# Kernel optimization log

Hardware: AMD Instinct MI355X
Metric: run time of the kernel (lower is better)

The kernel has to match this reference:

```python
import jax, jax.numpy as jnp
import numpy as np
from jax import lax

G = 8      # deform groups (weight groups == offset groups)
K = 3      # kernel size
K2 = K * K


def conv3x3(x, w, b):
    # NCHW, 3x3, stride 1, padding 1 (SAME)
    y = lax.conv_general_dilated(x, w, (1, 1), 'SAME',
                                 dimension_numbers=('NCHW', 'OIHW', 'NCHW'))
    return y + b[None, :, None, None]


def deform_conv2d(ref, offsets, w, b):
    # ref: [B,C,H,W], offsets: [B,2*G*K2,H,W] (torchvision layout: per group,
    # per kernel position, (dy, dx) pairs), w: [C_out, C_in/G, K, K], b: [C_out]
    B, C, H, W = ref.shape
    Cg = C // G
    off = offsets.reshape(B, G, K2, 2, H, W)
    dy = off[:, :, :, 0]  # [B,G,K2,H,W]
    dx = off[:, :, :, 1]
    ky = (jnp.arange(K2) // K - K // 2).astype(ref.dtype)  # kernel y offsets (pad=1)
    kx = (jnp.arange(K2) % K - K // 2).astype(ref.dtype)
    base_y = jnp.arange(H, dtype=ref.dtype)[:, None] + ky[:, None, None]  # [K2,H,1]
    base_x = jnp.arange(W, dtype=ref.dtype)[None, :] + kx[:, None, None]  # [K2,1,W]
    py = dy + base_y  # [B,G,K2,H,W]
    px = dx + base_x

    y0 = jnp.floor(py).astype(jnp.int32)
    x0 = jnp.floor(px).astype(jnp.int32)
    ly = py - y0.astype(ref.dtype)
    lx = px - x0.astype(ref.dtype)

    ref_flat = ref.reshape(B, G, Cg, H * W)

    def gather(yi, xi):
        valid = (yi >= 0) & (yi < H) & (xi >= 0) & (xi < W)
        idx = jnp.clip(yi, 0, H - 1) * W + jnp.clip(xi, 0, W - 1)  # [B,G,K2,H,W]
        vals = jnp.take_along_axis(ref_flat, idx.reshape(B, G, 1, K2 * H * W), axis=3)
        vals = vals.reshape(B, G, Cg, K2, H, W)
        return vals * valid[:, :, None].astype(ref.dtype)

    w00 = ((1 - ly) * (1 - lx))[:, :, None]
    w01 = ((1 - ly) * lx)[:, :, None]
    w10 = (ly * (1 - lx))[:, :, None]
    w11 = (ly * lx)[:, :, None]
    sampled = (w00 * gather(y0, x0) + w01 * gather(y0, x0 + 1)
               + w10 * gather(y0 + 1, x0) + w11 * gather(y0 + 1, x0 + 1))
    # grouped accumulation: weight [C_out, Cg, K, K] -> [G, OCg, Cg, K2]
    wg = w.reshape(G, C // G, Cg, K2)
    out = jnp.einsum('bgikhw,goik->bgohw', sampled, wg)
    return out.reshape(B, C, H, W) + b[None, :, None, None]


def setup_inputs() -> dict:
    key = jax.random.key(0)
    ks = jax.random.split(key, 10)
    B, C, H, W = 2, 64, 256, 256
    s64 = 1.0 / np.sqrt(C * 9)
    s128 = 1.0 / np.sqrt(128 * 9)
    return {
        'offset': jax.random.normal(ks[0], (B, C, H, W), jnp.float32),
        'ref': jax.random.normal(ks[1], (B, C, H, W), jnp.float32),
        'w_off': jax.random.normal(ks[2], (2 * K2 * G, C, K, K), jnp.float32) * s64,
        'b_off': jnp.zeros((2 * K2 * G,), jnp.float32),
        'w_def': jax.random.normal(ks[3], (C, C // G, K, K), jnp.float32) * (1.0 / np.sqrt((C // G) * 9)),
        'b_def': jnp.zeros((C,), jnp.float32),
        'w_r1': jax.random.normal(ks[4], (C, 2 * C, K, K), jnp.float32) * s128,
        'b_r1': jnp.zeros((C,), jnp.float32),
        'w_r2': jax.random.normal(ks[5], (C, C, K, K), jnp.float32) * s64,
        'b_r2': jnp.zeros((C,), jnp.float32),
    }


def reference(offset, ref, w_off, b_off, w_def, b_def, w_r1, b_r1, w_r2, b_r2):
    deform_offsets = conv3x3(offset, w_off, b_off)              # [B,144,H,W]
    aligned_ref = deform_conv2d(ref, deform_offsets, w_def, b_def)
    x = jnp.concatenate([ref, aligned_ref], axis=1)             # [B,128,H,W]
    x = jax.nn.relu(conv3x3(x, w_r1, b_r1))
    x = jax.nn.relu(conv3x3(x, w_r2, b_r2))
    return x + aligned_ref
```

## Files before the change

### kernel.cpp

```cpp
#include <hip/hip_runtime.h>

typedef __attribute__((ext_vector_type(8)))  short  short8;
typedef __attribute__((ext_vector_type(4)))  float  float4v;
typedef __attribute__((ext_vector_type(16))) float  float16v;

constexpr int HH = 256, WW = 256;
constexpr int PD = 258;
constexpr size_t HWsz = (size_t)HH * WW;

__device__ inline unsigned short f2bf(float f) {
    unsigned int u = __builtin_bit_cast(unsigned int, f);
    u += 0x7FFFu + ((u >> 16) & 1u);
    return (unsigned short)(u >> 16);
}
__device__ inline float bfhalf(unsigned int w, int hi) {
    return __builtin_bit_cast(float, hi ? (w & 0xFFFF0000u) : (w << 16));
}

template<int CDST, bool WRITE_G>
__global__ __launch_bounds__(256) void nchw_to_nhwc(
    const float* __restrict__ src, unsigned short* __restrict__ dst,
    unsigned short* __restrict__ dst_g)
{
    const int px = threadIdx.x, h = blockIdx.x, bi = blockIdx.y;
    const float* s = src + (size_t)bi * 64 * HWsz + (size_t)h * WW + px;
    unsigned short* d = dst + (((size_t)bi * PD + (h + 1)) * PD + (px + 1)) * CDST;
#pragma unroll
    for (int cg = 0; cg < 8; ++cg) {
        float v[8];
#pragma unroll
        for (int j = 0; j < 8; ++j) v[j] = s[(size_t)(cg * 8 + j) * HWsz];
        uint4 pk;
        pk.x = f2bf(v[0]) | ((unsigned)f2bf(v[1]) << 16);
        pk.y = f2bf(v[2]) | ((unsigned)f2bf(v[3]) << 16);
        pk.z = f2bf(v[4]) | ((unsigned)f2bf(v[5]) << 16);
        pk.w = f2bf(v[6]) | ((unsigned)f2bf(v[7]) << 16);
        *(uint4*)&d[cg * 8] = pk;
        if (WRITE_G) {
            unsigned short* dg = dst_g +
                (((size_t)(bi * 8 + cg) * HWsz) + (size_t)h * WW + px) * 8;
            *(uint4*)dg = pk;
        }
    }
}

__global__ __launch_bounds__(256) void zero_border(
    unsigned short* __restrict__ p_off, unsigned short* __restrict__ p_cat,
    unsigned short* __restrict__ p_x1)
{
    const int bi = blockIdx.y, which = blockIdx.z;
    unsigned short* buf = which == 0 ? p_off : (which == 1 ? p_cat : p_x1);
    const int CIN = (which == 1) ? 128 : 64;
    const int NG = CIN / 8;
    unsigned short* p = buf + (size_t)bi * PD * PD * CIN;
    const int total = 1028 * 16;
    for (int i = blockIdx.x * 256 + threadIdx.x; i < total; i += gridDim.x * 256) {
        int g = i & 15;
        if (g >= NG) continue;
        int pxi = i >> 4;
        int r, c;
        if (pxi < 258)       { r = 0;   c = pxi; }
        else if (pxi < 516)  { r = 257; c = pxi - 258; }
        else if (pxi < 772)  { r = pxi - 516 + 1; c = 0; }
        else                 { r = pxi - 772 + 1; c = 257; }
        uint4 z = {0, 0, 0, 0};
        *(uint4*)&p[((size_t)r * PD + c) * CIN + g * 8] = z;
    }
}

__device__ inline void pack_one(const float* __restrict__ w, short* __restrict__ wpk,
                                int Cout, int Cin, int e)
{
    int j = e & 7;
    int lane = (e >> 3) & 63;
    int ksp = 9 * (Cin / 16);
    int kstep = (e >> 9) % ksp;
    int cot = (e >> 9) / ksp;
    int tap = kstep / (Cin / 16);
    int ci = (kstep % (Cin / 16)) * 16 + (lane >> 5) * 8 + j;
    int co = cot * 32 + (lane & 31);
    float v = (co < Cout) ? w[((size_t)co * Cin + ci) * 9 + tap] : 0.f;
    wpk[e] = (short)f2bf(v);
}

__global__ __launch_bounds__(256) void pack_all(
    const float* __restrict__ w1, short* __restrict__ d1,
    const float* __restrict__ w2, short* __restrict__ d2,
    const float* __restrict__ w3, short* __restrict__ d3)
{
    int e = blockIdx.x * 256 + threadIdx.x;
    if (e < 110592)               pack_one(w1, d1, 144, 64, e);
    else if (e < 110592 + 73728)  pack_one(w2, d2, 64, 128, e - 110592);
    else if (e < 221184)          pack_one(w3, d3, 64, 64,  e - 184320);
}

template<int CIN, int COF, int COTB, int MODE, int MINW>
__global__ __launch_bounds__(256, MINW) void conv_mfma_nb(
    const unsigned short* __restrict__ src,
    const short* __restrict__ wpk,
    const float* __restrict__ bias,
    unsigned short* __restrict__ dst_bf,
    float* __restrict__ dst_f,
    const unsigned short* __restrict__ resid_bf)
{
    constexpr int CHUNKS = CIN / 32;
    constexpr int KST = 9 * (CIN / 16);
    constexpr int WSEG = 3 * 4 * 66 * 8;

    __shared__ unsigned short lds[4 * WSEG];

    const int tid  = threadIdx.x;
    const int lane = tid & 63;
    const int wv   = tid >> 6;
    const int half = lane >> 5;
    const int n32  = lane & 31;
    const int h  = blockIdx.x;
    const int bi = blockIdx.y / COTB;
    const int cb = blockIdx.y % COTB;
    const int cbase = cb * COF * 32;

    unsigned short* my = lds + wv * WSEG;
    const unsigned short* srcB = src + (size_t)bi * PD * PD * CIN;
    const short8* wbase = (const short8*)wpk;

    float16v acc[COF][2];
#pragma unroll
    for (int f = 0; f < COF; ++f) {
        float16v bv;
#pragma unroll
        for (int reg = 0; reg < 16; ++reg) {
            int co = cbase + f * 32 + (reg >> 2) * 8 + 4 * half + (reg & 3);
            float b = 0.f;
            if (MODE != 0 || co < 144) b = bias[co];
            bv[reg] = b;
        }
        acc[f][0] = bv;
        acc[f][1] = bv;
    }

    for (int ch = 0; ch < CHUNKS; ++ch) {
        const unsigned short* gband = srcB + ((size_t)h * PD + wv * 64) * CIN + ch * 32;
#pragma unroll
        for (int i0 = 0; i0 < 264; i0 += 64) {
            int i = i0 + lane;
            if (i0 + 64 > 264 && i >= 264) continue;
            int px = i >> 2, o = i & 3;
#pragma unroll
            for (int r = 0; r < 3; ++r) {
                uint4 v = *(const uint4*)(gband + ((size_t)r * PD + px) * CIN + o * 8);
                *(uint4*)&my[(((size_t)r * 4 + o) * 66 + px) * 8] = v;
            }
        }

#pragma unroll
        for (int tap = 0; tap < 9; ++tap) {
            const int row = tap / 3, dxo = tap % 3;
#pragma unroll
            for (int s = 0; s < 2; ++s) {
                const int kstep = tap * (CIN / 16) + ch * 2 + s;
                short8 a[COF];
#pragma unroll
                for (int f = 0; f < COF; ++f)
                    a[f] = wbase[((size_t)(cb * COF + f) * KST + kstep) * 64 + lane];
#pragma unroll
                for (int nt = 0; nt < 2; ++nt) {
                    short8 b = *(const short8*)
                        &my[(((size_t)row * 4 + s * 2 + half) * 66 + nt * 32 + dxo + n32) * 8];
#pragma unroll
                    for (int f = 0; f < COF; ++f)
                        acc[f][nt] = __builtin_amdgcn_mfma_f32_32x32x16_bf16(a[f], b, acc[f][nt], 0, 0, 0);
                }
            }
        }
    }

#pragma unroll
    for (int f = 0; f < COF; ++f) {
#pragma unroll
        for (int nt = 0; nt < 2; ++nt) {
            const int px = wv * 64 + nt * 32 + n32;
            float16v a = acc[f][nt];
#pragma unroll
            for (int q = 0; q < 4; ++q) {
                const int co4 = cbase + f * 32 + q * 8 + 4 * half;
                float v0 = a[q * 4 + 0], v1 = a[q * 4 + 1];
                float v2 = a[q * 4 + 2], v3 = a[q * 4 + 3];
                if (MODE == 0) {
                    if (co4 < 144) {
                        unsigned short* d = dst_bf + (size_t)bi * HWsz * 144;
                        uint2 pk;
                        pk.x = f2bf(v0) | ((unsigned)f2bf(v1) << 16);
                        pk.y = f2bf(v2) | ((unsigned)f2bf(v3) << 16);
                        *(uint2*)&d[((size_t)h * WW + px) * 144 + co4] = pk;
                    }
                } else if (MODE == 1) {
                    unsigned short* d = dst_bf + (size_t)bi * PD * PD * 64;
                    uint2 pk;
                    pk.x = f2bf(fmaxf(v0, 0.f)) | ((unsigned)f2bf(fmaxf(v1, 0.f)) << 16);
                    pk.y = f2bf(fmaxf(v2, 0.f)) | ((unsigned)f2bf(fmaxf(v3, 0.f)) << 16);
                    *(uint2*)&d[(((size_t)h + 1) * PD + (px + 1)) * 64 + co4] = pk;
                } else {
                    const unsigned short* rp = resid_bf + (size_t)bi * PD * PD * 128;
                    uint2 rv = *(const uint2*)&rp[(((size_t)h + 1) * PD + (px + 1)) * 128 + 64 + co4];
                    float r0 = bfhalf(rv.x, 0), r1 = bfhalf(rv.x, 1);
                    float r2 = bfhalf(rv.y, 0), r3 = bfhalf(rv.y, 1);
                    float* d = dst_f + (size_t)bi * 64 * HWsz + (size_t)h * WW + px;
                    d[(size_t)(co4 + 0) * HWsz] = fmaxf(v0, 0.f) + r0;
                    d[(size_t)(co4 + 1) * HWsz] = fmaxf(v1, 0.f) + r1;
                    d[(size_t)(co4 + 2) * HWsz] = fmaxf(v2, 0.f) + r2;
                    d[(size_t)(co4 + 3) * HWsz] = fmaxf(v3, 0.f) + r3;
                }
            }
        }
    }
}

__global__ __launch_bounds__(256) void deform_k6(
    const unsigned short* __restrict__ refg,
    const unsigned short* __restrict__ doff,
    const float* __restrict__ wdef, const float* __restrict__ bdef,
    unsigned short* __restrict__ pcat_out)
{
    __shared__ float wsm2[576];
    const int L = blockIdx.x;
    const int xcd = L & 7;
    const int j = L >> 3;
    const int g = j & 7;
    const int r = (j >> 3) & 31;
    const int bi = j >> 8;
    const int h = xcd * 32 + r;
    const int px = threadIdx.x;

    for (int i = threadIdx.x; i < 576; i += 256) {
        int o = i & 7, c = (i >> 3) & 7, k = i >> 6;
        wsm2[i] = wdef[(size_t)g * 576 + o * 72 + c * 9 + k];
    }
    __syncthreads();

    const unsigned int* dp = (const unsigned int*)(
        doff + (((size_t)bi * HWsz) + (size_t)h * WW + px) * 144 + g * 18);
    unsigned int dw[9];
#pragma unroll
    for (int k = 0; k < 9; ++k) dw[k] = dp[k];

    float2 acc2[4];
#pragma unroll
    for (int o = 0; o < 4; ++o)
        acc2[o] = make_float2(bdef[g * 8 + 2 * o], bdef[g * 8 + 2 * o + 1]);

    const unsigned short* rb = refg + (size_t)(bi * 8 + g) * HWsz * 8;

#pragma unroll
    for (int k = 0; k < 9; ++k) {
        float dy = bfhalf(dw[k], 0);
        float dx = bfhalf(dw[k], 1);
        float py = dy + (float)(h + k / 3 - 1);
        float pxs = dx + (float)(px + k % 3 - 1);
        float fy = floorf(py), fx = floorf(pxs);
        int y0 = (int)fy, x0i = (int)fx;
        float ly = py - fy, lx = pxs - fx;
        int y1 = y0 + 1, x1i = x0i + 1;
        bool vy0 = (y0 >= 0) & (y0 < HH), vy1 = (y1 >= 0) & (y1 < HH);
        bool vx0 = (x0i >= 0) & (x0i < WW), vx1 = (x1i >= 0) & (x1i < WW);
        int cy0 = min(max(y0, 0), HH - 1), cy1 = min(max(y1, 0), HH - 1);
        int cx0 = min(max(x0i, 0), WW - 1), cx1 = min(max(x1i, 0), WW - 1);
        float w00 = (1.f - ly) * (1.f - lx), w01 = (1.f - ly) * lx;
        float w10 = ly * (1.f - lx), w11 = ly * lx;
        if (!(vy0 && vx0)) w00 = 0.f;
        if (!(vy0 && vx1)) w01 = 0.f;
        if (!(vy1 && vx0)) w10 = 0.f;
        if (!(vy1 && vx1)) w11 = 0.f;

        uint4 q00 = *(const uint4*)(rb + ((size_t)cy0 * WW + cx0) * 8);
        uint4 q01 = *(const uint4*)(rb + ((size_t)cy0 * WW + cx1) * 8);
        uint4 q10 = *(const uint4*)(rb + ((size_t)cy1 * WW + cx0) * 8);
        uint4 q11 = *(const uint4*)(rb + ((size_t)cy1 * WW + cx1) * 8);
        union U { uint4 v; unsigned int a[4]; };
        U u00{q00}, u01{q01}, u10{q10}, u11{q11};

#pragma unroll
        for (int cw = 0; cw < 4; ++cw) {
#pragma unroll
            for (int hl = 0; hl < 2; ++hl) {
                int c = cw * 2 + hl;
                float sv = w00 * bfhalf(u00.a[cw], hl) + w01 * bfhalf(u01.a[cw], hl)
                         + w10 * bfhalf(u10.a[cw], hl) + w11 * bfhalf(u11.a[cw], hl);
                const float2* wp2 = (const float2*)&wsm2[((k * 8) + c) * 8];
#pragma unroll
                for (int o = 0; o < 4; ++o) {
                    acc2[o].x = fmaf(wp2[o].x, sv, acc2[o].x);
                    acc2[o].y = fmaf(wp2[o].y, sv, acc2[o].y);
                }
            }
        }
    }

    unsigned short* po = pcat_out + (((size_t)bi * PD + (h + 1)) * PD + (px + 1)) * 128 + 64 + g * 8;
    uint4 pk;
    pk.x = f2bf(acc2[0].x) | ((unsigned)f2bf(acc2[0].y) << 16);
    pk.y = f2bf(acc2[1].x) | ((unsigned)f2bf(acc2[1].y) << 16);
    pk.z = f2bf(acc2[2].x) | ((unsigned)f2bf(acc2[2].y) << 16);
    pk.w = f2bf(acc2[3].x) | ((unsigned)f2bf(acc2[3].y) << 16);
    *(uint4*)po = pk;
}

extern "C" void kernel_launch(void* const* d_in, const int* in_sizes, int n_in,
                              void* d_out, int out_size, void* d_ws, size_t ws_size,
                              hipStream_t stream)
{
    const float* offset = (const float*)d_in[0];
    const float* ref    = (const float*)d_in[1];
    const float* w_off  = (const float*)d_in[2];
    const float* b_off  = (const float*)d_in[3];
    const float* w_def  = (const float*)d_in[4];
    const float* b_def  = (const float*)d_in[5];
    const float* w_r1   = (const float*)d_in[6];
    const float* b_r1   = (const float*)d_in[7];
    const float* w_r2   = (const float*)d_in[8];
    const float* b_r2   = (const float*)d_in[9];
    float* out = (float*)d_out;

    unsigned short* p_off = (unsigned short*)d_ws;
    unsigned short* p_cat = p_off + (size_t)8520192;
    unsigned short* p_x1  = p_cat + (size_t)17040384;
    unsigned short* doff  = p_x1 + (size_t)8520192;
    unsigned short* refg  = doff + (size_t)18874368;
    short* wpk1  = (short*)(refg + (size_t)8388608);
    short* wpkr1 = wpk1 + 110592;
    short* wpkr2 = wpkr1 + 73728;

    zero_border<<<dim3(65, 2, 3), 256, 0, stream>>>(p_off, p_cat, p_x1);

    pack_all<<<dim3((221184 + 255) / 256), 256, 0, stream>>>(
        w_off, wpk1, w_r1, wpkr1, w_r2, wpkr2);

    nchw_to_nhwc<64, false><<<dim3(256, 2), 256, 0, stream>>>(offset, p_off, nullptr);
    nchw_to_nhwc<128, true><<<dim3(256, 2), 256, 0, stream>>>(ref, p_cat, refg);

    conv_mfma_nb<64, 2, 3, 0, 3><<<dim3(256, 6), 256, 0, stream>>>(
        p_off, wpk1, b_off, doff, nullptr, nullptr);

    deform_k6<<<dim3(4096), 256, 0, stream>>>(refg, doff, w_def, b_def, p_cat);

    conv_mfma_nb<128, 2, 1, 1, 3><<<dim3(256, 2), 256, 0, stream>>>(
        p_cat, wpkr1, b_r1, p_x1, nullptr, nullptr);

    conv_mfma_nb<64, 2, 1, 2, 3><<<dim3(256, 2), 256, 0, stream>>>(
        p_x1, wpkr2, b_r2, nullptr, out, p_cat);
}
```

Before: 345.0 us.

## Pad grouped ref buffer with zero border and vectorize deform bilinear math

Stores the per-group ref copy in a 260x260 zero-padded layout, zeroed by an extra zero_border slice. The deform kernel then clamps sample positions to [-1,256] and reads the four corners straight from the padded buffer, with no per-corner validity masks or index clamps. It also rewrites the bilinear blend and weight accumulation with two-wide float vector FMAs so the compiler can emit packed FP32 instructions. Clamping to -1 or 256 keeps the fractional weights, which still lands on zero padding, but the padding must stay zeroed or results go wrong.

```diff
diff --git a/kernel.cpp b/kernel.cpp
--- a/kernel.cpp
+++ b/kernel.cpp
@@ -3,9 +3,11 @@
 typedef __attribute__((ext_vector_type(8)))  short  short8;
 typedef __attribute__((ext_vector_type(4)))  float  float4v;
 typedef __attribute__((ext_vector_type(16))) float  float16v;
+typedef __attribute__((ext_vector_type(2)))  float  f32x2;
 
 constexpr int HH = 256, WW = 256;
 constexpr int PD = 258;
+constexpr int PR = 260;
 constexpr size_t HWsz = (size_t)HH * WW;
 
 __device__ inline unsigned short f2bf(float f) {
@@ -16,6 +18,13 @@
 __device__ inline float bfhalf(unsigned int w, int hi) {
     return __builtin_bit_cast(float, hi ? (w & 0xFFFF0000u) : (w << 16));
 }
+__device__ inline f32x2 unpk2(unsigned int w) {
+    f32x2 r;
+    r.x = __builtin_bit_cast(float, w << 16);
+    r.y = __builtin_bit_cast(float, w & 0xFFFF0000u);
+    return r;
+}
+__device__ inline f32x2 splat2(float s) { f32x2 r; r.x = s; r.y = s; return r; }
 
 template<int CDST, bool WRITE_G>
 __global__ __launch_bounds__(256) void nchw_to_nhwc(
@@ -38,7 +47,7 @@
         *(uint4*)&d[cg * 8] = pk;
         if (WRITE_G) {
             unsigned short* dg = dst_g +
-                (((size_t)(bi * 8 + cg) * HWsz) + (size_t)h * WW + px) * 8;
+                ((size_t)(bi * 8 + cg) * PR * PR + (size_t)(h + 1) * PR + (px + 1)) * 8;
             *(uint4*)dg = pk;
         }
     }
@@ -46,9 +55,21 @@
 
 __global__ __launch_bounds__(256) void zero_border(
     unsigned short* __restrict__ p_off, unsigned short* __restrict__ p_cat,
-    unsigned short* __restrict__ p_x1)
+    unsigned short* __restrict__ p_x1, unsigned short* __restrict__ refg)
 {
     const int bi = blockIdx.y, which = blockIdx.z;
+    if (which == 3) {
+        const int total = 8 * 1548;
+        for (int i = blockIdx.x * 256 + threadIdx.x; i < total; i += gridDim.x * 256) {
+            int g = i / 1548, t = i - g * 1548;
+            int r, c;
+            if (t < 780)  { int rr = t / 260; c = t - rr * 260; r = rr == 0 ? 0 : 256 + rr; }
+            else          { int u = t - 780; int cc = u >> 8; r = 1 + (u & 255); c = cc == 0 ? 0 : 256 + cc; }
+            uint4 z = {0, 0, 0, 0};
+            *(uint4*)&refg[((size_t)(bi * 8 + g) * PR * PR + (size_t)r * PR + c) * 8] = z;
+        }
+        return;
+    }
     unsigned short* buf = which == 0 ? p_off : (which == 1 ? p_cat : p_x1);
     const int CIN = (which == 1) ? 128 : 64;
     const int NG = CIN / 8;
@@ -215,7 +236,7 @@
     }
 }
 
-__global__ __launch_bounds__(256) void deform_k6(
+__global__ __launch_bounds__(256) void deform_k7(
     const unsigned short* __restrict__ refg,
     const unsigned short* __restrict__ doff,
     const float* __restrict__ wdef, const float* __restrict__ bdef,
@@ -243,54 +264,53 @@
 #pragma unroll
     for (int k = 0; k < 9; ++k) dw[k] = dp[k];
 
-    float2 acc2[4];
-#pragma unroll
-    for (int o = 0; o < 4; ++o)
-        acc2[o] = make_float2(bdef[g * 8 + 2 * o], bdef[g * 8 + 2 * o + 1]);
-
-    const unsigned short* rb = refg + (size_t)(bi * 8 + g) * HWsz * 8;
+    f32x2 acc2[4];
+#pragma unroll
+    for (int o = 0; o < 4; ++o) {
+        acc2[o].x = bdef[g * 8 + 2 * o];
+        acc2[o].y = bdef[g * 8 + 2 * o + 1];
+    }
+
+    const unsigned short* rb = refg + (size_t)(bi * 8 + g) * PR * PR * 8;
+    const float hf = (float)h, pxf = (float)px;
 
 #pragma unroll
     for (int k = 0; k < 9; ++k) {
         float dy = bfhalf(dw[k], 0);
         float dx = bfhalf(dw[k], 1);
-        float py = dy + (float)(h + k / 3 - 1);
-        float pxs = dx + (float)(px + k % 3 - 1);
+        float py  = dy + (hf + (float)(k / 3 - 1));
+        float pxs = dx + (pxf + (float)(k % 3 - 1));
+        py  = fminf(fmaxf(py,  -1.f), 256.f);
+        pxs = fminf(fmaxf(pxs, -1.f), 256.f);
         float fy = floorf(py), fx = floorf(pxs);
-        int y0 = (int)fy, x0i = (int)fx;
         float ly = py - fy, lx = pxs - fx;
-        int y1 = y0 + 1, x1i = x0i + 1;
-        bool vy0 = (y0 >= 0) & (y0 < HH), vy1 = (y1 >= 0) & (y1 < HH);
-        bool vx0 = (x0i >= 0) & (x0i < WW), vx1 = (x1i >= 0) & (x1i < WW);
-        int cy0 = min(max(y0, 0), HH - 1), cy1 = min(max(y1, 0), HH - 1);
-        int cx0 = min(max(x0i, 0), WW - 1), cx1 = min(max(x1i, 0), WW - 1);
-        float w00 = (1.f - ly) * (1.f - lx), w01 = (1.f - ly) * lx;
-        float w10 = ly * (1.f - lx), w11 = ly * lx;
-        if (!(vy0 && vx0)) w00 = 0.f;
-        if (!(vy0 && vx1)) w01 = 0.f;
-        if (!(vy1 && vx0)) w10 = 0.f;
-        if (!(vy1 && vx1)) w11 = 0.f;
-
-        uint4 q00 = *(const uint4*)(rb + ((size_t)cy0 * WW + cx0) * 8);
-        uint4 q01 = *(const uint4*)(rb + ((size_t)cy0 * WW + cx1) * 8);
-        uint4 q10 = *(const uint4*)(rb + ((size_t)cy1 * WW + cx0) * 8);
-        uint4 q11 = *(const uint4*)(rb + ((size_t)cy1 * WW + cx1) * 8);
+        int y0 = (int)fy, x0 = (int)fx;
+        int i00 = (y0 + 1) * PR + (x0 + 1);
+        float omly = 1.f - ly, omlx = 1.f - lx;
+        f32x2 w00 = splat2(omly * omlx), w01 = splat2(omly * lx);
+        f32x2 w10 = splat2(ly * omlx),  w11 = splat2(ly * lx);
+
+        const uint4 q00 = *(const uint4*)(rb + (size_t)i00 * 8);
+        const uint4 q01 = *(const uint4*)(rb + (size_t)(i00 + 1) * 8);
+        const uint4 q10 = *(const uint4*)(rb + (size_t)(i00 + PR) * 8);
+        const uint4 q11 = *(const uint4*)(rb + (size_t)(i00 + PR + 1) * 8);
         union U { uint4 v; unsigned int a[4]; };
         U u00{q00}, u01{q01}, u10{q10}, u11{q11};
 
 #pragma unroll
         for (int cw = 0; cw < 4; ++cw) {
-#pragma unroll
-            for (int hl = 0; hl < 2; ++hl) {
-                int c = cw * 2 + hl;
-                float sv = w00 * bfhalf(u00.a[cw], hl) + w01 * bfhalf(u01.a[cw], hl)
-                         + w10 * bfhalf(u10.a[cw], hl) + w11 * bfhalf(u11.a[cw], hl);
-                const float2* wp2 = (const float2*)&wsm2[((k * 8) + c) * 8];
-#pragma unroll
-                for (int o = 0; o < 4; ++o) {
-                    acc2[o].x = fmaf(wp2[o].x, sv, acc2[o].x);
-                    acc2[o].y = fmaf(wp2[o].y, sv, acc2[o].y);
-                }
+            f32x2 sv = unpk2(u00.a[cw]) * w00;
+            sv = __builtin_elementwise_fma(unpk2(u01.a[cw]), w01, sv);
+            sv = __builtin_elementwise_fma(unpk2(u10.a[cw]), w10, sv);
+            sv = __builtin_elementwise_fma(unpk2(u11.a[cw]), w11, sv);
+            f32x2 bx = splat2(sv.x);
+            f32x2 by = splat2(sv.y);
+            const f32x2* wpa = (const f32x2*)&wsm2[((k * 8) + cw * 2) * 8];
+            const f32x2* wpb = (const f32x2*)&wsm2[((k * 8) + cw * 2 + 1) * 8];
+#pragma unroll
+            for (int o = 0; o < 4; ++o) {
+                acc2[o] = __builtin_elementwise_fma(wpa[o], bx, acc2[o]);
+                acc2[o] = __builtin_elementwise_fma(wpb[o], by, acc2[o]);
             }
         }
     }
@@ -325,11 +345,11 @@
     unsigned short* p_x1  = p_cat + (size_t)17040384;
     unsigned short* doff  = p_x1 + (size_t)8520192;
     unsigned short* refg  = doff + (size_t)18874368;
-    short* wpk1  = (short*)(refg + (size_t)8388608);
+    short* wpk1  = (short*)(refg + (size_t)8652800);
     short* wpkr1 = wpk1 + 110592;
     short* wpkr2 = wpkr1 + 73728;
 
-    zero_border<<<dim3(65, 2, 3), 256, 0, stream>>>(p_off, p_cat, p_x1);
+    zero_border<<<dim3(65, 2, 4), 256, 0, stream>>>(p_off, p_cat, p_x1, refg);
 
     pack_all<<<dim3((221184 + 255) / 256), 256, 0, stream>>>(
         w_off, wpk1, w_r1, wpkr1, w_r2, wpkr2);
@@ -340,7 +360,7 @@
     conv_mfma_nb<64, 2, 3, 0, 3><<<dim3(256, 6), 256, 0, stream>>>(
         p_off, wpk1, b_off, doff, nullptr, nullptr);
 
-    deform_k6<<<dim3(4096), 256, 0, stream>>>(refg, doff, w_def, b_def, p_cat);
+    deform_k7<<<dim3(4096), 256, 0, stream>>>(refg, doff, w_def, b_def, p_cat);
 
     conv_mfma_nb<128, 2, 1, 1, 3><<<dim3(256, 2), 256, 0, stream>>>(
         p_cat, wpkr1, b_r1, p_x1, nullptr, nullptr);
```

Result: faster. 336.4 us (-2.5%).
